# Performance work log

Measured on AMD Instinct MI355X. Metric: run time of the kernel, lower is better.

The kernel has to match this reference:

```python
import jax, jax.numpy as jnp
import numpy as np


def setup_inputs() -> dict:
    key = jax.random.key(0)
    ks = jax.random.split(key, 8)
    Bsz, Dm, L, N = 2, 2048, 1024, 16
    u = jax.random.normal(ks[0], (Bsz, Dm, L), jnp.float32)
    delta = jax.random.normal(ks[1], (Bsz, Dm, L), jnp.float32) * 0.5
    # A is negative in Mamba (stable decay); keep values O(1) negative
    A = -jnp.exp(jax.random.normal(ks[2], (Dm, N), jnp.float32) * 0.5)
    B = jax.random.normal(ks[3], (Bsz, N, L), jnp.float32)
    C = jax.random.normal(ks[4], (Bsz, N, L), jnp.float32)
    D = jax.random.normal(ks[5], (Dm,), jnp.float32)
    z = jax.random.normal(ks[6], (Bsz, Dm, L), jnp.float32)
    delta_bias = jax.random.normal(ks[7], (Dm,), jnp.float32) * 0.1
    return {"u": u, "delta": delta, "A": A, "B": B, "C": C,
            "D": D, "z": z, "delta_bias": delta_bias, "delta_softplus": 1}


def reference(u, delta, A, B, C, D, z, delta_bias, delta_softplus):
    # u, delta, z: (Bsz, Dm, L); A: (Dm, N); B, C: (Bsz, N, L)
    dt = delta + delta_bias[None, :, None]
    if delta_softplus:
        dt = jax.nn.softplus(dt)

    # move scan (length) axis to the front
    dt_l = jnp.moveaxis(dt, -1, 0)   # (L, Bsz, Dm)
    u_l = jnp.moveaxis(u, -1, 0)     # (L, Bsz, Dm)
    B_l = jnp.moveaxis(B, -1, 0)     # (L, Bsz, N)
    C_l = jnp.moveaxis(C, -1, 0)     # (L, Bsz, N)

    def step(x, inp):
        dti, ui, Bi, Ci = inp
        dA = jnp.exp(dti[..., None] * A)                  # (Bsz, Dm, N)
        dBu = (dti * ui)[..., None] * Bi[:, None, :]      # (Bsz, Dm, N)
        x = dA * x + dBu
        y = jnp.einsum('bdn,bn->bd', x, Ci)               # (Bsz, Dm)
        return x, y

    x0 = jnp.zeros((u.shape[0], u.shape[1], A.shape[1]), dtype=u.dtype)
    _, ys = jax.lax.scan(step, x0, (dt_l, u_l, B_l, C_l))  # ys: (L, Bsz, Dm)
    y = jnp.moveaxis(ys, 0, -1)                            # (Bsz, Dm, L)
    y = y + u * D[None, :, None]
    y = y * (z * jax.nn.sigmoid(z))  # silu gate
    return y
```

## Files before the change

kernel.cpp:

```cpp
#include <hip/hip_runtime.h>
#include <math.h>

constexpr int Bsz = 2, Dm = 2048, L = 1024, N = 16;
constexpr int CL = 16;
constexpr int WPR = 2;
constexpr int RPB = 4;
constexpr int TPB = RPB * WPR * 64;
constexpr int ISTR2 = 65;
constexpr int LROW2 = CL * ISTR2;
constexpr int TI = 2;
constexpr int NT = CL / TI;
constexpr float LOG2E = 1.4426950408889634f;
constexpr float RLOG2E = 0.6931471805599453f;

#define EXP2(x) __builtin_amdgcn_exp2f(x)
#define TOFF(il, cg, k) ((il) * 256 + (cg) * 4 + ((k) ^ (((cg) >> 1) & 3)))

__global__ __launch_bounds__(256) void transform_bc_kernel(
    const float* __restrict__ B_g, const float* __restrict__ C_g,
    float4* __restrict__ Bs, float4* __restrict__ Cs)
{
    const int o = threadIdx.x + 256 * blockIdx.x;
    const int b = blockIdx.y;
    const float* __restrict__ src = blockIdx.z ? C_g : B_g;
    float4* __restrict__ dst = blockIdx.z ? Cs : Bs;
    const int k = o & 3, cg = (o >> 2) & 63, i = o >> 8;
    const int l = cg * CL + i;
    float4 v;
    v.x = src[(size_t)(b * N + 4 * k + 0) * L + l];
    v.y = src[(size_t)(b * N + 4 * k + 1) * L + l];
    v.z = src[(size_t)(b * N + 4 * k + 2) * L + l];
    v.w = src[(size_t)(b * N + 4 * k + 3) * L + l];
    dst[(size_t)b * 4096 + o] = v;
}

template<bool XF>
__global__ __launch_bounds__(TPB) void mamba_scan16_kernel(
    const float* __restrict__ u_g, const float* __restrict__ delta_g,
    const float* __restrict__ A_g,
    const float* __restrict__ B_g, const float* __restrict__ C_g,
    const float4* __restrict__ Bs, const float4* __restrict__ Cs,
    const float* __restrict__ D_g, const float* __restrict__ z_g,
    const float* __restrict__ bias_g, const int* __restrict__ sp_g,
    float* __restrict__ y_g)
{
    __shared__ float2 du_s[RPB * LROW2];
    __shared__ float4 tb[2][TI * 256];
    __shared__ float xw_s[RPB][16];

    const int tid = threadIdx.x;
    const int wid = tid >> 6;
    const int lane = tid & 63;
    const int W = wid & 1;
    const int r = wid >> 1;
    const int h = lane >> 5;
    const int c = lane & 31;
    const int cg = W * 32 + c;
    const int row = blockIdx.x * RPB + r;
    const int b = row >> 11;
    const int d = row & (Dm - 1);
    const int sp = sp_g[0];
    const float bias = bias_g[d];
    const int lb = r * LROW2;
    const int t128 = tid & 127;
    const int stg = TOFF(tid >> 8, (tid >> 2) & 63, tid & 3);
    const size_t Bb = (size_t)b * 4096;

    float4 sB, sC;
    if (XF) sB = Bs[Bb + tid];

#pragma unroll
    for (int p = 0; p < 2; ++p) {
        const int l0 = 4 * t128 + 512 * p;
        const size_t gb = (size_t)row * L + l0;
        const float4 d4 = *reinterpret_cast<const float4*>(&delta_g[gb]);
        const float4 u4 = *reinterpret_cast<const float4*>(&u_g[gb]);
        const float dv[4] = {d4.x, d4.y, d4.z, d4.w};
        const float uv[4] = {u4.x, u4.y, u4.z, u4.w};
#pragma unroll
        for (int k = 0; k < 4; ++k) {
            const int li = l0 + k;
            const float t = dv[k] + bias;
            const float e = EXP2(-fabsf(t) * LOG2E);
            const float p_ = sp ? (fmaxf(t, 0.f) +
                                   __builtin_amdgcn_logf(1.f + e) * RLOG2E)
                                : t;
            const int a = (li & (CL - 1)) * ISTR2 + (li >> 4);
            du_s[lb + a] = make_float2(p_, uv[k]);
        }
    }
    if (XF) tb[0][stg] = sB;
    __syncthreads();

    float A2[8];
#pragma unroll
    for (int g = 0; g < 2; ++g) {
        const float4 a4 = *reinterpret_cast<const float4*>(&A_g[d * N + h * 8 + g * 4]);
        A2[g * 4 + 0] = a4.x * LOG2E; A2[g * 4 + 1] = a4.y * LOG2E;
        A2[g * 4 + 2] = a4.z * LOG2E; A2[g * 4 + 3] = a4.w * LOG2E;
    }
    const int k0 = 2 * h;
    const float Dd = D_g[d];

    float x[8];
#pragma unroll
    for (int n = 0; n < 8; ++n) x[n] = 0.f;
    float ssum = 0.f;

    if (XF) {
#pragma unroll 1
        for (int t = 0; t < NT; ++t) {
            if (t + 1 < NT) sB = Bs[Bb + (t + 1) * 512 + tid];
#pragma unroll
            for (int il = 0; il < TI; ++il) {
                const int i = t * TI + il;
                const float2 du = du_s[lb + i * ISTR2 + cg];
                const float dtp = du.x;
                const float dtu = du.x * du.y;
                ssum += dtp;
                const float4 B0 = tb[t & 1][TOFF(il, cg, k0)];
                const float4 B1 = tb[t & 1][TOFF(il, cg, k0 + 1)];
                const float bv[8] = {B0.x, B0.y, B0.z, B0.w, B1.x, B1.y, B1.z, B1.w};
#pragma unroll
                for (int n = 0; n < 8; ++n) {
                    const float a = EXP2(dtp * A2[n]);
                    x[n] = fmaf(a, x[n], dtu * bv[n]);
                }
            }
            if (t + 1 < NT) tb[(t + 1) & 1][stg] = sB;
            __syncthreads();
        }
    } else {
#pragma unroll 4
        for (int i = 0; i < CL; ++i) {
            const float2 du = du_s[lb + i * ISTR2 + cg];
            const float dtp = du.x;
            const float dtu = du.x * du.y;
            ssum += dtp;
            const int l = cg * CL + i;
            float4 B0, B1;
#pragma unroll
            for (int q = 0; q < 4; ++q) {
                (&B0.x)[q] = B_g[(size_t)(b * N + 4 * k0 + q) * L + l];
                (&B1.x)[q] = B_g[(size_t)(b * N + 4 * k0 + 4 + q) * L + l];
            }
            const float bv[8] = {B0.x, B0.y, B0.z, B0.w, B1.x, B1.y, B1.z, B1.w};
#pragma unroll
            for (int n = 0; n < 8; ++n) {
                const float a = EXP2(dtp * A2[n]);
                x[n] = fmaf(a, x[n], dtu * bv[n]);
            }
        }
    }

    if (XF) { sB = Bs[Bb + tid]; sC = Cs[Bb + tid]; }

    float P[8];
#pragma unroll
    for (int n = 0; n < 8; ++n) P[n] = EXP2(A2[n] * ssum);
#pragma unroll
    for (int s = 1; s < 32; s <<= 1) {
        const bool ok = (c >= s);
#pragma unroll
        for (int n = 0; n < 8; ++n) {
            const float xp = __shfl_up(x[n], s, 32);
            const float Pp = __shfl_up(P[n], s, 32);
            if (ok) {
                x[n] = fmaf(P[n], xp, x[n]);
                P[n] = P[n] * Pp;
            }
        }
    }

    if (W == 0 && c == 31) {
#pragma unroll
        for (int n = 0; n < 8; ++n) xw_s[r][h * 8 + n] = x[n];
    }
    if (XF) { tb[0][stg] = sB; tb[1][stg] = sC; }
    __syncthreads();

    float xt[8];
#pragma unroll
    for (int n = 0; n < 8; ++n) xt[n] = xw_s[r][h * 8 + n];
#pragma unroll
    for (int n = 0; n < 8; ++n) {
        const float xi = __shfl_up(x[n], 1, 32);
        const float Pi = __shfl_up(P[n], 1, 32);
        const float xe = (c == 0) ? 0.f : xi;
        const float Pe = (c == 0) ? 1.f : Pi;
        x[n] = W ? fmaf(Pe, xt[n], xe) : xe;
    }

    if (XF) {
#pragma unroll 1
        for (int t = 0; t < NT; ++t) {
            if (t + 1 < NT) {
                sB = Bs[Bb + (t + 1) * 512 + tid];
                sC = Cs[Bb + (t + 1) * 512 + tid];
            }
#pragma unroll
            for (int il = 0; il < TI; ++il) {
                const int i = t * TI + il;
                const float2 du = du_s[lb + i * ISTR2 + cg];
                const float dtp = du.x;
                const float uu = du.y;
                const float dtu = dtp * uu;
                const float4 B0 = tb[0][TOFF(il, cg, k0)];
                const float4 B1 = tb[0][TOFF(il, cg, k0 + 1)];
                const float4 C0 = tb[1][TOFF(il, cg, k0)];
                const float4 C1 = tb[1][TOFF(il, cg, k0 + 1)];
                const float bv[8] = {B0.x, B0.y, B0.z, B0.w, B1.x, B1.y, B1.z, B1.w};
                const float cv[8] = {C0.x, C0.y, C0.z, C0.w, C1.x, C1.y, C1.z, C1.w};
                float acc = 0.f;
#pragma unroll
                for (int n = 0; n < 8; ++n) {
                    const float a = EXP2(dtp * A2[n]);
                    x[n] = fmaf(a, x[n], dtu * bv[n]);
                    acc = fmaf(x[n], cv[n], acc);
                }
                acc += __shfl_xor(acc, 32, 64);
                if (h == 0)
                    du_s[lb + i * ISTR2 + cg].x = fmaf(uu, Dd, acc);
            }
            __syncthreads();
            if (t + 1 < NT) {
                tb[0][stg] = sB;
                tb[1][stg] = sC;
                __syncthreads();
            }
        }
    } else {
#pragma unroll 4
        for (int i = 0; i < CL; ++i) {
            const float2 du = du_s[lb + i * ISTR2 + cg];
            const float dtp = du.x;
            const float uu = du.y;
            const float dtu = dtp * uu;
            const int l = cg * CL + i;
            float4 B0, B1, C0, C1;
#pragma unroll
            for (int q = 0; q < 4; ++q) {
                (&B0.x)[q] = B_g[(size_t)(b * N + 4 * k0 + q) * L + l];
                (&B1.x)[q] = B_g[(size_t)(b * N + 4 * k0 + 4 + q) * L + l];
                (&C0.x)[q] = C_g[(size_t)(b * N + 4 * k0 + q) * L + l];
                (&C1.x)[q] = C_g[(size_t)(b * N + 4 * k0 + 4 + q) * L + l];
            }
            const float bv[8] = {B0.x, B0.y, B0.z, B0.w, B1.x, B1.y, B1.z, B1.w};
            const float cv[8] = {C0.x, C0.y, C0.z, C0.w, C1.x, C1.y, C1.z, C1.w};
            float acc = 0.f;
#pragma unroll
            for (int n = 0; n < 8; ++n) {
                const float a = EXP2(dtp * A2[n]);
                x[n] = fmaf(a, x[n], dtu * bv[n]);
                acc = fmaf(x[n], cv[n], acc);
            }
            acc += __shfl_xor(acc, 32, 64);
            if (h == 0)
                du_s[lb + i * ISTR2 + cg].x = fmaf(uu, Dd, acc);
        }
        __syncthreads();
    }

#pragma unroll
    for (int p = 0; p < 2; ++p) {
        const int l0 = 4 * t128 + 512 * p;
        const size_t gb = (size_t)row * L + l0;
        const float4 z4 = *reinterpret_cast<const float4*>(&z_g[gb]);
        const float zv[4] = {z4.x, z4.y, z4.z, z4.w};
        float out[4];
#pragma unroll
        for (int k = 0; k < 4; ++k) {
            const int li = l0 + k;
            const float yc = du_s[lb + (li & (CL - 1)) * ISTR2 + (li >> 4)].x;
            const float e = EXP2(-zv[k] * LOG2E);
            const float sig = __builtin_amdgcn_rcpf(1.f + e);
            out[k] = yc * (zv[k] * sig);
        }
        *reinterpret_cast<float4*>(&y_g[gb]) = make_float4(out[0], out[1], out[2], out[3]);
    }
}

extern "C" void kernel_launch(void* const* d_in, const int* in_sizes, int n_in,
                              void* d_out, int out_size, void* d_ws, size_t ws_size,
                              hipStream_t stream) {
    const float* u     = (const float*)d_in[0];
    const float* delta = (const float*)d_in[1];
    const float* A     = (const float*)d_in[2];
    const float* B     = (const float*)d_in[3];
    const float* C     = (const float*)d_in[4];
    const float* D     = (const float*)d_in[5];
    const float* z     = (const float*)d_in[6];
    const float* bias  = (const float*)d_in[7];
    const int*   sp    = (const int*)d_in[8];
    float* y = (float*)d_out;

    const size_t bc_bytes = (size_t)Bsz * 4096 * sizeof(float4);
    const bool xf = ws_size >= 2 * bc_bytes;
    float4* Bs = (float4*)d_ws;
    float4* Cs = (float4*)((char*)d_ws + bc_bytes);

    if (xf) {
        transform_bc_kernel<<<dim3(16, Bsz, 2), 256, 0, stream>>>(B, C, Bs, Cs);
        mamba_scan16_kernel<true><<<dim3((Bsz * Dm) / RPB), TPB, 0, stream>>>(
            u, delta, A, B, C, Bs, Cs, D, z, bias, sp, y);
    } else {
        mamba_scan16_kernel<false><<<dim3((Bsz * Dm) / RPB), TPB, 0, stream>>>(
            u, delta, A, B, C, Bs, Cs, D, z, bias, sp, y);
    }
}
```

Baseline: 49.41 us.

## Keep per-chunk dt/u in registers and double-buffer B/C tiles in pass two

After: 64.32 us. +30.2%, slower.

```diff
diff --git a/kernel.cpp b/kernel.cpp
--- a/kernel.cpp
+++ b/kernel.cpp
@@ -6,8 +6,6 @@
 constexpr int WPR = 2;
 constexpr int RPB = 4;
 constexpr int TPB = RPB * WPR * 64;
-constexpr int ISTR2 = 65;
-constexpr int LROW2 = CL * ISTR2;
 constexpr int TI = 2;
 constexpr int NT = CL / TI;
 constexpr float LOG2E = 1.4426950408889634f;
@@ -35,7 +33,7 @@
 }
 
 template<bool XF>
-__global__ __launch_bounds__(TPB) void mamba_scan16_kernel(
+__global__ __launch_bounds__(TPB) void mamba_scan17_kernel(
     const float* __restrict__ u_g, const float* __restrict__ delta_g,
     const float* __restrict__ A_g,
     const float* __restrict__ B_g, const float* __restrict__ C_g,
@@ -44,8 +42,8 @@
     const float* __restrict__ bias_g, const int* __restrict__ sp_g,
     float* __restrict__ y_g)
 {
-    __shared__ float2 du_s[RPB * LROW2];
-    __shared__ float4 tb[2][TI * 256];
+    __shared__ float4 tbB[2][TI * 256];
+    __shared__ float4 tbC[2][TI * 256];
     __shared__ float xw_s[RPB][16];
 
     const int tid = threadIdx.x;
@@ -59,39 +57,33 @@
     const int row = blockIdx.x * RPB + r;
     const int b = row >> 11;
     const int d = row & (Dm - 1);
-    const int sp = sp_g[0];
-    const float bias = bias_g[d];
-    const int lb = r * LROW2;
-    const int t128 = tid & 127;
     const int stg = TOFF(tid >> 8, (tid >> 2) & 63, tid & 3);
     const size_t Bb = (size_t)b * 4096;
+    const int k0 = 2 * h;
 
     float4 sB, sC;
     if (XF) sB = Bs[Bb + tid];
 
-#pragma unroll
-    for (int p = 0; p < 2; ++p) {
-        const int l0 = 4 * t128 + 512 * p;
-        const size_t gb = (size_t)row * L + l0;
-        const float4 d4 = *reinterpret_cast<const float4*>(&delta_g[gb]);
-        const float4 u4 = *reinterpret_cast<const float4*>(&u_g[gb]);
-        const float dv[4] = {d4.x, d4.y, d4.z, d4.w};
-        const float uv[4] = {u4.x, u4.y, u4.z, u4.w};
-#pragma unroll
-        for (int k = 0; k < 4; ++k) {
-            const int li = l0 + k;
-            const float t = dv[k] + bias;
-            const float e = EXP2(-fabsf(t) * LOG2E);
-            const float p_ = sp ? (fmaxf(t, 0.f) +
-                                   __builtin_amdgcn_logf(1.f + e) * RLOG2E)
-                                : t;
-            const int a = (li & (CL - 1)) * ISTR2 + (li >> 4);
-            du_s[lb + a] = make_float2(p_, uv[k]);
-        }
-    }
-    if (XF) tb[0][stg] = sB;
-    __syncthreads();
-
+    const size_t gch = (size_t)row * L + cg * CL;
+    float dt[CL], uu[CL];
+    {
+        const float bias = bias_g[d];
+        const int sp = sp_g[0];
+#pragma unroll
+        for (int p = 0; p < 4; ++p) {
+            const float4 d4 = *reinterpret_cast<const float4*>(&delta_g[gch + 4 * p]);
+            const float4 u4 = *reinterpret_cast<const float4*>(&u_g[gch + 4 * p]);
+#pragma unroll
+            for (int k = 0; k < 4; ++k) {
+                const float t = (&d4.x)[k] + bias;
+                const float e = EXP2(-fabsf(t) * LOG2E);
+                dt[4 * p + k] = sp ? (fmaxf(t, 0.f) +
+                                      __builtin_amdgcn_logf(1.f + e) * RLOG2E)
+                                   : t;
+                uu[4 * p + k] = (&u4.x)[k];
+            }
+        }
+    }
     float A2[8];
 #pragma unroll
     for (int g = 0; g < 2; ++g) {
@@ -99,8 +91,8 @@
         A2[g * 4 + 0] = a4.x * LOG2E; A2[g * 4 + 1] = a4.y * LOG2E;
         A2[g * 4 + 2] = a4.z * LOG2E; A2[g * 4 + 3] = a4.w * LOG2E;
     }
-    const int k0 = 2 * h;
-    const float Dd = D_g[d];
+    if (XF) tbB[0][stg] = sB;
+    __syncthreads();
 
     float x[8];
 #pragma unroll
@@ -108,18 +100,17 @@
     float ssum = 0.f;
 
     if (XF) {
-#pragma unroll 1
+#pragma unroll
         for (int t = 0; t < NT; ++t) {
             if (t + 1 < NT) sB = Bs[Bb + (t + 1) * 512 + tid];
 #pragma unroll
             for (int il = 0; il < TI; ++il) {
                 const int i = t * TI + il;
-                const float2 du = du_s[lb + i * ISTR2 + cg];
-                const float dtp = du.x;
-                const float dtu = du.x * du.y;
+                const float dtp = dt[i];
+                const float dtu = dtp * uu[i];
                 ssum += dtp;
-                const float4 B0 = tb[t & 1][TOFF(il, cg, k0)];
-                const float4 B1 = tb[t & 1][TOFF(il, cg, k0 + 1)];
+                const float4 B0 = tbB[t & 1][TOFF(il, cg, k0)];
+                const float4 B1 = tbB[t & 1][TOFF(il, cg, k0 + 1)];
                 const float bv[8] = {B0.x, B0.y, B0.z, B0.w, B1.x, B1.y, B1.z, B1.w};
 #pragma unroll
                 for (int n = 0; n < 8; ++n) {
@@ -127,15 +118,14 @@
                     x[n] = fmaf(a, x[n], dtu * bv[n]);
                 }
             }
-            if (t + 1 < NT) tb[(t + 1) & 1][stg] = sB;
+            if (t + 1 < NT) tbB[(t + 1) & 1][stg] = sB;
             __syncthreads();
         }
     } else {
-#pragma unroll 4
+#pragma unroll
         for (int i = 0; i < CL; ++i) {
-            const float2 du = du_s[lb + i * ISTR2 + cg];
-            const float dtp = du.x;
-            const float dtu = du.x * du.y;
+            const float dtp = dt[i];
+            const float dtu = dtp * uu[i];
             ssum += dtp;
             const int l = cg * CL + i;
             float4 B0, B1;
@@ -176,7 +166,7 @@
 #pragma unroll
         for (int n = 0; n < 8; ++n) xw_s[r][h * 8 + n] = x[n];
     }
-    if (XF) { tb[0][stg] = sB; tb[1][stg] = sC; }
+    if (XF) { tbB[0][stg] = sB; tbC[0][stg] = sC; }
     __syncthreads();
 
     float xt[8];
@@ -191,8 +181,9 @@
         x[n] = W ? fmaf(Pe, xt[n], xe) : xe;
     }
 
+    const float Dd = D_g[d];
     if (XF) {
-#pragma unroll 1
+#pragma unroll
         for (int t = 0; t < NT; ++t) {
             if (t + 1 < NT) {
                 sB = Bs[Bb + (t + 1) * 512 + tid];
@@ -201,14 +192,12 @@
 #pragma unroll
             for (int il = 0; il < TI; ++il) {
                 const int i = t * TI + il;
-                const float2 du = du_s[lb + i * ISTR2 + cg];
-                const float dtp = du.x;
-                const float uu = du.y;
-                const float dtu = dtp * uu;
-                const float4 B0 = tb[0][TOFF(il, cg, k0)];
-                const float4 B1 = tb[0][TOFF(il, cg, k0 + 1)];
-                const float4 C0 = tb[1][TOFF(il, cg, k0)];
-                const float4 C1 = tb[1][TOFF(il, cg, k0 + 1)];
+                const float dtp = dt[i];
+                const float dtu = dtp * uu[i];
+                const float4 B0 = tbB[t & 1][TOFF(il, cg, k0)];
+                const float4 B1 = tbB[t & 1][TOFF(il, cg, k0 + 1)];
+                const float4 C0 = tbC[t & 1][TOFF(il, cg, k0)];
+                const float4 C1 = tbC[t & 1][TOFF(il, cg, k0 + 1)];
                 const float bv[8] = {B0.x, B0.y, B0.z, B0.w, B1.x, B1.y, B1.z, B1.w};
                 const float cv[8] = {C0.x, C0.y, C0.z, C0.w, C1.x, C1.y, C1.z, C1.w};
                 float acc = 0.f;
@@ -219,23 +208,19 @@
                     acc = fmaf(x[n], cv[n], acc);
                 }
                 acc += __shfl_xor(acc, 32, 64);
-                if (h == 0)
-                    du_s[lb + i * ISTR2 + cg].x = fmaf(uu, Dd, acc);
-            }
-            __syncthreads();
+                uu[i] = fmaf(uu[i], Dd, acc);
+            }
             if (t + 1 < NT) {
-                tb[0][stg] = sB;
-                tb[1][stg] = sC;
+                tbB[(t + 1) & 1][stg] = sB;
+                tbC[(t + 1) & 1][stg] = sC;
                 __syncthreads();
             }
         }
     } else {
-#pragma unroll 4
+#pragma unroll
         for (int i = 0; i < CL; ++i) {
-            const float2 du = du_s[lb + i * ISTR2 + cg];
-            const float dtp = du.x;
-            const float uu = du.y;
-            const float dtu = dtp * uu;
+            const float dtp = dt[i];
+            const float dtu = dtp * uu[i];
             const int l = cg * CL + i;
             float4 B0, B1, C0, C1;
 #pragma unroll
@@ -255,28 +240,27 @@
                 acc = fmaf(x[n], cv[n], acc);
             }
             acc += __shfl_xor(acc, 32, 64);
-            if (h == 0)
-                du_s[lb + i * ISTR2 + cg].x = fmaf(uu, Dd, acc);
-        }
-        __syncthreads();
-    }
-
-#pragma unroll
-    for (int p = 0; p < 2; ++p) {
-        const int l0 = 4 * t128 + 512 * p;
-        const size_t gb = (size_t)row * L + l0;
-        const float4 z4 = *reinterpret_cast<const float4*>(&z_g[gb]);
-        const float zv[4] = {z4.x, z4.y, z4.z, z4.w};
-        float out[4];
-#pragma unroll
-        for (int k = 0; k < 4; ++k) {
-            const int li = l0 + k;
-            const float yc = du_s[lb + (li & (CL - 1)) * ISTR2 + (li >> 4)].x;
-            const float e = EXP2(-zv[k] * LOG2E);
+            uu[i] = fmaf(uu[i], Dd, acc);
+        }
+    }
+
+    {
+        const size_t gz = gch + h * 8;
+        const float4 z0 = *reinterpret_cast<const float4*>(&z_g[gz]);
+        const float4 z1 = *reinterpret_cast<const float4*>(&z_g[gz + 4]);
+        float out[8];
+#pragma unroll
+        for (int j = 0; j < 8; ++j) {
+            const float zv = (j < 4) ? (&z0.x)[j] : (&z1.x)[j - 4];
+            const float yc = h ? uu[8 + j] : uu[j];
+            const float e = EXP2(-zv * LOG2E);
             const float sig = __builtin_amdgcn_rcpf(1.f + e);
-            out[k] = yc * (zv[k] * sig);
-        }
-        *reinterpret_cast<float4*>(&y_g[gb]) = make_float4(out[0], out[1], out[2], out[3]);
+            out[j] = yc * (zv * sig);
+        }
+        *reinterpret_cast<float4*>(&y_g[gz]) =
+            make_float4(out[0], out[1], out[2], out[3]);
+        *reinterpret_cast<float4*>(&y_g[gz + 4]) =
+            make_float4(out[4], out[5], out[6], out[7]);
     }
 }
 
@@ -301,10 +285,10 @@
 
     if (xf) {
         transform_bc_kernel<<<dim3(16, Bsz, 2), 256, 0, stream>>>(B, C, Bs, Cs);
-        mamba_scan16_kernel<true><<<dim3((Bsz * Dm) / RPB), TPB, 0, stream>>>(
+        mamba_scan17_kernel<true><<<dim3((Bsz * Dm) / RPB), TPB, 0, stream>>>(
             u, delta, A, B, C, Bs, Cs, D, z, bias, sp, y);
     } else {
-        mamba_scan16_kernel<false><<<dim3((Bsz * Dm) / RPB), TPB, 0, stream>>>(
+        mamba_scan17_kernel<false><<<dim3((Bsz * Dm) / RPB), TPB, 0, stream>>>(
             u, delta, A, B, C, Bs, Cs, D, z, bias, sp, y);
     }
 }
```

## Relayout staged B/C tiles as padded float2 rows and keep outputs in registers

Applied to the files above, without the earlier changes.

Result: no change. 49.58 us (median of 2 runs) (+0.3%).

```diff
diff --git a/kernel.cpp b/kernel.cpp
--- a/kernel.cpp
+++ b/kernel.cpp
@@ -6,15 +6,15 @@
 constexpr int WPR = 2;
 constexpr int RPB = 4;
 constexpr int TPB = RPB * WPR * 64;
+constexpr int TI = 2;
+constexpr int NT = CL / TI;
 constexpr int ISTR2 = 65;
 constexpr int LROW2 = CL * ISTR2;
-constexpr int TI = 2;
-constexpr int NT = CL / TI;
+constexpr int TS2 = 8 * 65;
 constexpr float LOG2E = 1.4426950408889634f;
 constexpr float RLOG2E = 0.6931471805599453f;
 
 #define EXP2(x) __builtin_amdgcn_exp2f(x)
-#define TOFF(il, cg, k) ((il) * 256 + (cg) * 4 + ((k) ^ (((cg) >> 1) & 3)))
 
 __global__ __launch_bounds__(256) void transform_bc_kernel(
     const float* __restrict__ B_g, const float* __restrict__ C_g,
@@ -24,7 +24,7 @@
     const int b = blockIdx.y;
     const float* __restrict__ src = blockIdx.z ? C_g : B_g;
     float4* __restrict__ dst = blockIdx.z ? Cs : Bs;
-    const int k = o & 3, cg = (o >> 2) & 63, i = o >> 8;
+    const int cg = o & 63, k = (o >> 6) & 3, i = o >> 8;
     const int l = cg * CL + i;
     float4 v;
     v.x = src[(size_t)(b * N + 4 * k + 0) * L + l];
@@ -35,7 +35,7 @@
 }
 
 template<bool XF>
-__global__ __launch_bounds__(TPB) void mamba_scan16_kernel(
+__global__ __launch_bounds__(TPB) void mamba_scan18_kernel(
     const float* __restrict__ u_g, const float* __restrict__ delta_g,
     const float* __restrict__ A_g,
     const float* __restrict__ B_g, const float* __restrict__ C_g,
@@ -45,7 +45,7 @@
     float* __restrict__ y_g)
 {
     __shared__ float2 du_s[RPB * LROW2];
-    __shared__ float4 tb[2][TI * 256];
+    __shared__ float2 tb2[2][TI * TS2];
     __shared__ float xw_s[RPB][16];
 
     const int tid = threadIdx.x;
@@ -59,12 +59,12 @@
     const int row = blockIdx.x * RPB + r;
     const int b = row >> 11;
     const int d = row & (Dm - 1);
-    const int sp = sp_g[0];
-    const float bias = bias_g[d];
+    const size_t Bb = (size_t)b * 4096;
     const int lb = r * LROW2;
     const int t128 = tid & 127;
-    const int stg = TOFF(tid >> 8, (tid >> 2) & 63, tid & 3);
-    const size_t Bb = (size_t)b * 4096;
+    const int stg0 = (wid >> 2) * TS2 + (2 * (wid & 3)) * 65 + lane;
+    const int stg1 = stg0 + 65;
+    const int trb = (4 * h) * 65 + cg;
 
     float4 sB, sC;
     if (XF) sB = Bs[Bb + tid];
@@ -75,23 +75,20 @@
         const size_t gb = (size_t)row * L + l0;
         const float4 d4 = *reinterpret_cast<const float4*>(&delta_g[gb]);
         const float4 u4 = *reinterpret_cast<const float4*>(&u_g[gb]);
-        const float dv[4] = {d4.x, d4.y, d4.z, d4.w};
-        const float uv[4] = {u4.x, u4.y, u4.z, u4.w};
+        const float bias = bias_g[d];
+        const int sp = sp_g[0];
 #pragma unroll
         for (int k = 0; k < 4; ++k) {
             const int li = l0 + k;
-            const float t = dv[k] + bias;
+            const float t = (&d4.x)[k] + bias;
             const float e = EXP2(-fabsf(t) * LOG2E);
             const float p_ = sp ? (fmaxf(t, 0.f) +
                                    __builtin_amdgcn_logf(1.f + e) * RLOG2E)
                                 : t;
             const int a = (li & (CL - 1)) * ISTR2 + (li >> 4);
-            du_s[lb + a] = make_float2(p_, uv[k]);
-        }
-    }
-    if (XF) tb[0][stg] = sB;
-    __syncthreads();
-
+            du_s[lb + a] = make_float2(p_, (&u4.x)[k]);
+        }
+    }
     float A2[8];
 #pragma unroll
     for (int g = 0; g < 2; ++g) {
@@ -99,16 +96,19 @@
         A2[g * 4 + 0] = a4.x * LOG2E; A2[g * 4 + 1] = a4.y * LOG2E;
         A2[g * 4 + 2] = a4.z * LOG2E; A2[g * 4 + 3] = a4.w * LOG2E;
     }
-    const int k0 = 2 * h;
-    const float Dd = D_g[d];
-
-    float x[8];
-#pragma unroll
-    for (int n = 0; n < 8; ++n) x[n] = 0.f;
+    if (XF) {
+        tb2[0][stg0] = make_float2(sB.x, sB.y);
+        tb2[0][stg1] = make_float2(sB.z, sB.w);
+    }
+    __syncthreads();
+
+    float x[8], y[8];
+#pragma unroll
+    for (int n = 0; n < 8; ++n) { x[n] = 0.f; y[n] = 0.f; }
     float ssum = 0.f;
 
     if (XF) {
-#pragma unroll 1
+#pragma unroll
         for (int t = 0; t < NT; ++t) {
             if (t + 1 < NT) sB = Bs[Bb + (t + 1) * 512 + tid];
 #pragma unroll
@@ -118,26 +118,34 @@
                 const float dtp = du.x;
                 const float dtu = du.x * du.y;
                 ssum += dtp;
-                const float4 B0 = tb[t & 1][TOFF(il, cg, k0)];
-                const float4 B1 = tb[t & 1][TOFF(il, cg, k0 + 1)];
-                const float bv[8] = {B0.x, B0.y, B0.z, B0.w, B1.x, B1.y, B1.z, B1.w};
+                const int rb = il * TS2 + trb;
+                const float2 q0 = tb2[t & 1][rb];
+                const float2 q1 = tb2[t & 1][rb + 65];
+                const float2 q2 = tb2[t & 1][rb + 130];
+                const float2 q3 = tb2[t & 1][rb + 195];
+                const float bv[8] = {q0.x, q0.y, q1.x, q1.y,
+                                     q2.x, q2.y, q3.x, q3.y};
 #pragma unroll
                 for (int n = 0; n < 8; ++n) {
                     const float a = EXP2(dtp * A2[n]);
                     x[n] = fmaf(a, x[n], dtu * bv[n]);
                 }
             }
-            if (t + 1 < NT) tb[(t + 1) & 1][stg] = sB;
+            if (t + 1 < NT) {
+                tb2[(t + 1) & 1][stg0] = make_float2(sB.x, sB.y);
+                tb2[(t + 1) & 1][stg1] = make_float2(sB.z, sB.w);
+            }
             __syncthreads();
         }
     } else {
-#pragma unroll 4
+#pragma unroll
         for (int i = 0; i < CL; ++i) {
             const float2 du = du_s[lb + i * ISTR2 + cg];
             const float dtp = du.x;
             const float dtu = du.x * du.y;
             ssum += dtp;
             const int l = cg * CL + i;
+            const int k0 = 2 * h;
             float4 B0, B1;
 #pragma unroll
             for (int q = 0; q < 4; ++q) {
@@ -176,7 +184,12 @@
 #pragma unroll
         for (int n = 0; n < 8; ++n) xw_s[r][h * 8 + n] = x[n];
     }
-    if (XF) { tb[0][stg] = sB; tb[1][stg] = sC; }
+    if (XF) {
+        tb2[0][stg0] = make_float2(sB.x, sB.y);
+        tb2[0][stg1] = make_float2(sB.z, sB.w);
+        tb2[1][stg0] = make_float2(sC.x, sC.y);
+        tb2[1][stg1] = make_float2(sC.z, sC.w);
+    }
     __syncthreads();
 
     float xt[8];
@@ -191,8 +204,9 @@
         x[n] = W ? fmaf(Pe, xt[n], xe) : xe;
     }
 
+    const float Dd = D_g[d];
     if (XF) {
-#pragma unroll 1
+#pragma unroll
         for (int t = 0; t < NT; ++t) {
             if (t + 1 < NT) {
                 sB = Bs[Bb + (t + 1) * 512 + tid];
@@ -205,12 +219,19 @@
                 const float dtp = du.x;
                 const float uu = du.y;
                 const float dtu = dtp * uu;
-                const float4 B0 = tb[0][TOFF(il, cg, k0)];
-                const float4 B1 = tb[0][TOFF(il, cg, k0 + 1)];
-                const float4 C0 = tb[1][TOFF(il, cg, k0)];
-                const float4 C1 = tb[1][TOFF(il, cg, k0 + 1)];
-                const float bv[8] = {B0.x, B0.y, B0.z, B0.w, B1.x, B1.y, B1.z, B1.w};
-                const float cv[8] = {C0.x, C0.y, C0.z, C0.w, C1.x, C1.y, C1.z, C1.w};
+                const int rb = il * TS2 + trb;
+                const float2 b0 = tb2[0][rb];
+                const float2 b1 = tb2[0][rb + 65];
+                const float2 b2 = tb2[0][rb + 130];
+                const float2 b3 = tb2[0][rb + 195];
+                const float2 c0 = tb2[1][rb];
+                const float2 c1 = tb2[1][rb + 65];
+                const float2 c2 = tb2[1][rb + 130];
+                const float2 c3 = tb2[1][rb + 195];
+                const float bv[8] = {b0.x, b0.y, b1.x, b1.y,
+                                     b2.x, b2.y, b3.x, b3.y};
+                const float cv[8] = {c0.x, c0.y, c1.x, c1.y,
+                                     c2.x, c2.y, c3.x, c3.y};
                 float acc = 0.f;
 #pragma unroll
                 for (int n = 0; n < 8; ++n) {
@@ -219,24 +240,27 @@
                     acc = fmaf(x[n], cv[n], acc);
                 }
                 acc += __shfl_xor(acc, 32, 64);
-                if (h == 0)
-                    du_s[lb + i * ISTR2 + cg].x = fmaf(uu, Dd, acc);
+                const float yv = fmaf(uu, Dd, acc);
+                y[i & 7] = ((i >> 3) == h) ? yv : y[i & 7];
             }
             __syncthreads();
             if (t + 1 < NT) {
-                tb[0][stg] = sB;
-                tb[1][stg] = sC;
+                tb2[0][stg0] = make_float2(sB.x, sB.y);
+                tb2[0][stg1] = make_float2(sB.z, sB.w);
+                tb2[1][stg0] = make_float2(sC.x, sC.y);
+                tb2[1][stg1] = make_float2(sC.z, sC.w);
                 __syncthreads();
             }
         }
     } else {
-#pragma unroll 4
+#pragma unroll
         for (int i = 0; i < CL; ++i) {
             const float2 du = du_s[lb + i * ISTR2 + cg];
             const float dtp = du.x;
             const float uu = du.y;
             const float dtu = dtp * uu;
             const int l = cg * CL + i;
+            const int k0 = 2 * h;
             float4 B0, B1, C0, C1;
 #pragma unroll
             for (int q = 0; q < 4; ++q) {
@@ -255,28 +279,27 @@
                 acc = fmaf(x[n], cv[n], acc);
             }
             acc += __shfl_xor(acc, 32, 64);
-            if (h == 0)
-                du_s[lb + i * ISTR2 + cg].x = fmaf(uu, Dd, acc);
-        }
-        __syncthreads();
-    }
-
-#pragma unroll
-    for (int p = 0; p < 2; ++p) {
-        const int l0 = 4 * t128 + 512 * p;
-        const size_t gb = (size_t)row * L + l0;
-        const float4 z4 = *reinterpret_cast<const float4*>(&z_g[gb]);
-        const float zv[4] = {z4.x, z4.y, z4.z, z4.w};
-        float out[4];
-#pragma unroll
-        for (int k = 0; k < 4; ++k) {
-            const int li = l0 + k;
-            const float yc = du_s[lb + (li & (CL - 1)) * ISTR2 + (li >> 4)].x;
-            const float e = EXP2(-zv[k] * LOG2E);
+            const float yv = fmaf(uu, Dd, acc);
+            y[i & 7] = ((i >> 3) == h) ? yv : y[i & 7];
+        }
+    }
+
+    {
+        const size_t gz = (size_t)row * L + cg * CL + h * 8;
+        const float4 z0 = *reinterpret_cast<const float4*>(&z_g[gz]);
+        const float4 z1 = *reinterpret_cast<const float4*>(&z_g[gz + 4]);
+        float out[8];
+#pragma unroll
+        for (int j = 0; j < 8; ++j) {
+            const float zv = (j < 4) ? (&z0.x)[j] : (&z1.x)[j - 4];
+            const float e = EXP2(-zv * LOG2E);
             const float sig = __builtin_amdgcn_rcpf(1.f + e);
-            out[k] = yc * (zv[k] * sig);
-        }
-        *reinterpret_cast<float4*>(&y_g[gb]) = make_float4(out[0], out[1], out[2], out[3]);
+            out[j] = y[j] * (zv * sig);
+        }
+        *reinterpret_cast<float4*>(&y_g[gz]) =
+            make_float4(out[0], out[1], out[2], out[3]);
+        *reinterpret_cast<float4*>(&y_g[gz + 4]) =
+            make_float4(out[4], out[5], out[6], out[7]);
     }
 }
 
@@ -301,10 +324,10 @@
 
     if (xf) {
         transform_bc_kernel<<<dim3(16, Bsz, 2), 256, 0, stream>>>(B, C, Bs, Cs);
-        mamba_scan16_kernel<true><<<dim3((Bsz * Dm) / RPB), TPB, 0, stream>>>(
+        mamba_scan18_kernel<true><<<dim3((Bsz * Dm) / RPB), TPB, 0, stream>>>(
             u, delta, A, B, C, Bs, Cs, D, z, bias, sp, y);
     } else {
-        mamba_scan16_kernel<false><<<dim3((Bsz * Dm) / RPB), TPB, 0, stream>>>(
+        mamba_scan18_kernel<false><<<dim3((Bsz * Dm) / RPB), TPB, 0, stream>>>(
             u, delta, A, B, C, Bs, Cs, D, z, bias, sp, y);
     }
 }
```
